# Kernel tuning notes

Hardware: AMD Instinct MI355X
Metric: run time of the kernel (lower is better)

Reference implementation:

```python
import jax, jax.numpy as jnp
import numpy as np

# Model dims (must match init_kwargs / input_specs)
D = 64          # hidden_dims
L = 2           # num_layer
R = 50          # num_relation
N_RAW = 20000   # num_nodes (module uses num_nodes+1 internally, node 0 = padding)
N = N_RAW + 1
A = 6           # max_arity
E = 30000       # num hyperedges
B = 4           # batch size
C = 500         # candidates per query (1 true + negatives, all differ in one slot)
ARITY = 4       # query arity (constant per batch, as the asserts require)
FEAT = 2 * D    # feature_dim = hidden_dims + input_dim
LN_EPS = 1e-5


def _sinusoidal_pos(max_arity, dim):
    # static_positional_encoding: frozen sinusoidal table, row 0 zeroed (padding)
    pos = np.arange(max_arity + 1, dtype=np.float64)[:, None]
    i = np.arange(dim, dtype=np.float64)[None, :]
    angle = pos / np.power(10000.0, (2.0 * np.floor(i / 2.0)) / dim)
    pe = np.where(np.arange(dim)[None, :] % 2 == 0, np.sin(angle), np.cos(angle))
    pe[0] = 0.0
    return jnp.asarray(pe, jnp.float32)


def setup_inputs() -> dict:
    key = jax.random.key(0)
    ks = jax.random.split(key, 16)
    # --- query batch: one corrupted slot per row, constant relation / arity per row ---
    base = jax.random.randint(ks[0], (B, A), 1, N)                       # entity ids 1..N-1
    base = base * (jnp.arange(A)[None, :] < ARITY)                       # pad slots >= arity -> node 0
    pos_corrupt = jax.random.randint(ks[1], (B,), 0, ARITY)              # which slot differs
    cand = (jnp.arange(C)[None, :] + jax.random.randint(ks[2], (B, 1), 1, N)) % (N - 1) + 1  # [B,C] distinct ids
    ent = jnp.broadcast_to(base[:, None, :], (B, C, A))
    entities_idx = jnp.where(jnp.arange(A)[None, None, :] == pos_corrupt[:, None, None],
                             cand[:, :, None], ent).astype(jnp.int64)    # [B,C,A]
    r_idx = jnp.broadcast_to(jax.random.randint(ks[3], (B, 1), 0, R), (B, C)).astype(jnp.int64)
    arity = jnp.full((B, C), ARITY, dtype=jnp.int64)
    # --- hypergraph: padded incidence lists ---
    edge_ar = jax.random.randint(ks[4], (E,), 2, A + 1)
    edge_list = (jax.random.randint(ks[5], (E, A), 1, N)
                 * (jnp.arange(A)[None, :] < edge_ar[:, None])).astype(jnp.int64)  # [E,A], 0-padded
    rel_list = jax.random.randint(ks[6], (E,), 0, R).astype(jnp.int64)
    # --- parameters ---
    sD = 1.0 / np.sqrt(D)
    sF = 1.0 / np.sqrt(FEAT)
    params = dict(
        query_emb=jax.random.normal(ks[7], (R, D), jnp.float32) * sD,
        rel_emb=jax.random.normal(ks[8], (L, R, D), jnp.float32) * sD,   # per-layer relation table (dependent=False)
        W_agg=jax.random.normal(ks[9], (L, D, D), jnp.float32) * sD,
        W_self=jax.random.normal(ks[10], (L, D, D), jnp.float32) * sD,
        b_lin=jnp.zeros((L, D), jnp.float32),
        ln_g=jnp.ones((L, D), jnp.float32),
        ln_b=jnp.zeros((L, D), jnp.float32),
        W1=jax.random.normal(ks[11], (FEAT, FEAT), jnp.float32) * sF,
        b1=jnp.zeros((FEAT,), jnp.float32),
        W2=jax.random.normal(ks[12], (FEAT, 1), jnp.float32) * sF,
        b2=jnp.zeros((1,), jnp.float32),
    )
    return dict(r_idx=r_idx, entities_idx=entities_idx, arity=arity,
                edge_list=edge_list, rel_list=rel_list,
                pos_table=_sinusoidal_pos(A, D), **params)


def _layer_norm(x, g, b):
    mu = x.mean(-1, keepdims=True)
    var = jnp.mean(jnp.square(x - mu), -1, keepdims=True)
    return (x - mu) * jax.lax.rsqrt(var + LN_EPS) * g + b


def reference(r_idx, entities_idx, arity, edge_list, rel_list, pos_table,
              query_emb, rel_emb, W_agg, W_self, b_lin, ln_g, ln_b, W1, b1, W2, b2):
    all_idx = jnp.transpose(entities_idx, (0, 2, 1))                 # [B,A,C]
    mask_for_diff = jnp.all(all_idx[:, :, :1] == all_idx, axis=-1)   # [B,A] True = slot constant
    pos_search = jnp.argmax(~mask_for_diff, axis=1)                  # [B] corrupted slot
    query = query_emb[r_idx[:, 0]]                                   # [B,D]

    rng = jnp.arange(A)
    valid = rng[None, :] < arity[:, :1]                              # [B,A]
    result = (valid & (rng[None, :] != pos_search[:, None])).astype(all_idx.dtype)  # [B,A]
    idx_ws = all_idx[:, :, 0] * result                               # [B,A] node ids (0 = skip)
    b_ix = jnp.arange(r_idx.shape[0])

    # init: scatter-add relation query + positional encodings onto the query entities
    init = jnp.zeros((r_idx.shape[0], N, D), jnp.float32)
    init = init.at[b_ix[:, None], idx_ws].add(
        jnp.broadcast_to(query[:, None, :], (r_idx.shape[0], A, D)))
    pos_src = pos_table[result * (rng + 1)[None, :]]                 # [B,A,D]
    init = init.at[b_ix[:, None], idx_ws].add(pos_src)
    init = init.at[:, 0, :].set(0.0)                                 # padding node stays 0

    ev = (edge_list != 0)                                            # [E,A] valid slots
    pos_e = pos_table[jnp.arange(1, A + 1)[None, :] * ev]            # [E,A,D] (pos_table[0]=0)
    evf = ev[None, :, :, None].astype(jnp.float32)

    layer_input = init
    for l in range(L):
        h_e = layer_input[:, edge_list]                              # [B,E,A,D] gather
        r_e = rel_emb[l][rel_list]                                   # [E,D]
        m = (h_e + pos_e[None]) * r_e[None, :, None, :] * evf        # per-slot message factor
        msg = (m.sum(axis=2, keepdims=True) - m) * evf               # sum over other slots j != i
        agg = jnp.zeros_like(layer_input).at[:, edge_list].add(msg)  # scatter-add to nodes
        agg = agg.at[:, 0, :].set(0.0)
        out = agg @ W_agg[l] + layer_input @ W_self[l] + b_lin[l]
        out = _layer_norm(out, ln_g[l], ln_b[l])                     # (dropout = identity at eval)
        hidden = jax.nn.relu(out)
        layer_input = hidden + layer_input                           # short_cut residual

    # gather candidate rows (exactly one differing slot per batch row -> jit-friendly)
    cand = jnp.take_along_axis(all_idx, pos_search[:, None, None], axis=1)[:, 0, :]  # [B,C]
    feat_nodes = layer_input[b_ix[:, None], cand]                    # [B,C,D]
    feat = jnp.concatenate(
        [feat_nodes, jnp.broadcast_to(query[:, None, :], feat_nodes.shape)], axis=-1)  # [B,C,2D]
    score = (jax.nn.relu(feat @ W1 + b1) @ W2 + b2)[..., 0]          # [B,C]
    return score
```

## Files before the change

### kernel.cpp

```cpp
#include <hip/hip_runtime.h>

#define D_ 64
#define L_ 2
#define R_ 50
#define N_ 20001
#define A_ 6
#define E_ 30000
#define B_ 4
#define C_ 500
#define FEAT_ 128
#define SC_CAP 8192
#define DCAP 64

__device__ __forceinline__ float rlane(float v, int k) {
  return __builtin_bit_cast(float, __builtin_amdgcn_readlane(__builtin_bit_cast(int, v), k));
}
__device__ __forceinline__ float wave_sum(float v) {
#pragma unroll
  for (int off = 32; off; off >>= 1) v += __shfl_xor(v, off);
  return v;
}
__device__ __forceinline__ float sel6(float p0, float p1, float p2, float p3,
                                      float p4, float p5, int a) {
  float r = p0;
  r = (a == 1) ? p1 : r; r = (a == 2) ? p2 : r; r = (a == 3) ? p3 : r;
  r = (a == 4) ? p4 : r; r = (a == 5) ? p5 : r;
  return r;
}


#define ZQUADS 15007

__global__ void zero_kernel(float4* __restrict__ z) {
  int i = blockIdx.x * blockDim.x + threadIdx.x;
  if (i < ZQUADS) z[i] = make_float4(0.f, 0.f, 0.f, 0.f);
}


#define IB_INIT 4
#define IB_EMASK ((E_ + 255) / 256)
#define IB_BUCKET ((E_ * A_ + 255) / 256)
#define IB_BLOCKS (IB_INIT + IB_EMASK + IB_BUCKET)

__global__ __launch_bounds__(256) void init_bucket_kernel(
    const int* __restrict__ r_idx, const int* __restrict__ ents,
    const int* __restrict__ arity, const float* __restrict__ pos_table,
    const float* __restrict__ query_emb, const int* __restrict__ edge_list,
    int* __restrict__ seednode, float* __restrict__ seedvec,
    int* __restrict__ dirtyA, int* __restrict__ dirty_n, int* __restrict__ meta,
    int* __restrict__ deg, int* __restrict__ bucket, int* __restrict__ emask) {
  __shared__ int diff[A_];
  int bid = blockIdx.x, t = threadIdx.x;
  if (bid < IB_INIT) {
    int b = bid;
    if (t < A_) diff[t] = 0;
    __syncthreads();
#pragma unroll
    for (int a = 0; a < A_; ++a) {
      int v0 = ents[(b * C_) * A_ + a];
      int dd = 0;
      for (int c = t; c < C_; c += 256) dd |= (ents[(b * C_ + c) * A_ + a] != v0);
      if (dd) diff[a] = 1;
    }
    __syncthreads();
    int ps = 0;
    for (int a = A_ - 1; a >= 0; --a) if (diff[a]) ps = a;
    int qr = r_idx[b * C_];
    if (t == 0) { meta[b] = ps; meta[B_ + b] = qr; }
    int ar = arity[b * C_];
    int lane = t & 63;
    for (int a = (t >> 6); a < A_; a += 4) {
      int slot = b * A_ + a;
      if (a < ar && a != ps) {
        int n = ents[(b * C_) * A_ + a];
        seedvec[slot * D_ + lane] = query_emb[qr * D_ + lane] + pos_table[(a + 1) * D_ + lane];
        if (lane == 0) {
          seednode[slot] = n;
          atomicOr(&dirtyA[n], 1 << b);
          atomicOr(&dirty_n[n], 1 << b);
        }
      } else {
        if (lane == 0) seednode[slot] = 0;
      }
    }
  } else if (bid < IB_INIT + IB_EMASK) {
    int e = (bid - IB_INIT) * 256 + t;
    if (e < E_) {
      int msk = 0;
#pragma unroll
      for (int a = 0; a < A_; ++a)
        if (edge_list[e * A_ + a]) msk |= 1 << a;
      emask[e] = msk;
    }
  } else {
    int i = (bid - IB_INIT - IB_EMASK) * 256 + t;
    if (i < E_ * A_) {
      int n = edge_list[i];
      if (n) {
        int slot = atomicAdd(&deg[n], 1);
        if (slot < DCAP) bucket[n * DCAP + slot] = i;
      }
    }
  }
}


#define MAIN_BLOCKS ((N_ + 31) / 32)
#define EPS_BLOCKS ((E_ + 3) / 4)

__global__ __launch_bounds__(256) void main_eps_kernel(
    const int* __restrict__ deg, const int* __restrict__ bucket,
    const int* __restrict__ edge_list, const int* __restrict__ rel_list,
    const int* __restrict__ emask,
    const float* __restrict__ pos_table, const float* __restrict__ rel_emb_l,
    float* __restrict__ H1,
    const float* __restrict__ Wa, const float* __restrict__ bl_,
    const float* __restrict__ g_, const float* __restrict__ be_,
    const int* __restrict__ dirtyA, int* __restrict__ dirty_n,
    const int* __restrict__ seednode, const float* __restrict__ seedvec,
    float* __restrict__ Scorr, unsigned short* __restrict__ emap,
    int* __restrict__ ctrs) {
  __shared__ float A_lds[32 * 68];
  __shared__ float B_lds[64 * 64];
  int t = threadIdx.x;
  int wv = t >> 6, l = t & 63;

  if (blockIdx.x >= MAIN_BLOCKS) {
    int e = (blockIdx.x - MAIN_BLOCKS) * 4 + wv;
    if (e >= E_) return;
    int mem[A_];
    int m = 0;
#pragma unroll
    for (int a = 0; a < A_; ++a) {
      mem[a] = edge_list[e * A_ + a];
      if (mem[a]) m |= dirtyA[mem[a]];
    }
    if (l == 0) *reinterpret_cast<unsigned long long*>(&emap[e * B_]) = 0ull;
    if (!m) return;
#pragma unroll
    for (int a = 0; a < A_; ++a)
      if (l == a && mem[a]) atomicOr(&dirty_n[mem[a]], m);
    float rel = rel_emb_l[rel_list[e] * D_ + l];
#pragma unroll
    for (int b = 0; b < B_; ++b) {
      if ((m >> b) & 1) {
        float s = 0.f;
#pragma unroll
        for (int a = 0; a < A_; ++a) {
          if (mem[a]) {
#pragma unroll
            for (int j = 0; j < A_; ++j) {
              int sl = b * A_ + j;
              if (seednode[sl] == mem[a]) s += seedvec[sl * D_ + l];
            }
          }
        }
        int slot = 0;
        if (l == 0) slot = atomicAdd(&ctrs[1], 1);
        slot = __shfl(slot, 0);
        if (slot < SC_CAP) {
          Scorr[slot * D_ + l] = rel * s;
          if (l == 0) emap[e * B_ + b] = (unsigned short)(slot + 1);
        }
      }
    }
    return;
  }

  int m0 = blockIdx.x * 32;
  int ty = t >> 4, tx = t & 15;

  float pv0 = pos_table[1 * D_ + l], pv1 = pos_table[2 * D_ + l];
  float pv2 = pos_table[3 * D_ + l], pv3 = pos_table[4 * D_ + l];
  float pv4 = pos_table[5 * D_ + l], pv5 = pos_table[6 * D_ + l];

#pragma unroll
  for (int it = 0; it < 4; ++it) {
    int idx = t + 256 * it;
    reinterpret_cast<float4*>(B_lds)[idx] = reinterpret_cast<const float4*>(Wa)[idx];
  }

  for (int q = 0; q < 8; ++q) {
    int li = wv * 8 + q;
    int n = m0 + li;
    float aggv = 0.f;
    if (n < N_) {
      int dg = __builtin_amdgcn_readfirstlane(deg[n]);
      int base = n * DCAP;
      for (int p = 0; p < dg; p += 8) {
        int cnt = dg - p;
        int idx8[8];
#pragma unroll
        for (int u = 0; u < 8; ++u) idx8[u] = (u < cnt) ? bucket[base + p + u] : -1;
#pragma unroll
        for (int u = 0; u < 8; ++u) {
          if (idx8[u] >= 0) {
            int e = idx8[u] / 6, a = idx8[u] - e * 6;
            int msk = emask[e];
            float rel = rel_emb_l[rel_list[e] * D_ + l];
            float possum = 0.f;
            possum += (msk & 1) ? pv0 : 0.f;
            possum += (msk & 2) ? pv1 : 0.f;
            possum += (msk & 4) ? pv2 : 0.f;
            possum += (msk & 8) ? pv3 : 0.f;
            possum += (msk & 16) ? pv4 : 0.f;
            possum += (msk & 32) ? pv5 : 0.f;
            float pa = sel6(pv0, pv1, pv2, pv3, pv4, pv5, a);
            aggv = fmaf(rel, possum - pa, aggv);
          }
        }
      }
    }
    A_lds[li * 68 + l] = aggv;
  }
  __syncthreads();

  float acc[2][4];
  float4 bl4 = *reinterpret_cast<const float4*>(&bl_[tx * 4]);
#pragma unroll
  for (int i = 0; i < 2; ++i) {
    acc[i][0] = bl4.x; acc[i][1] = bl4.y; acc[i][2] = bl4.z; acc[i][3] = bl4.w;
  }
#pragma unroll 8
  for (int k = 0; k < 64; ++k) {
    float4 b4 = *reinterpret_cast<const float4*>(&B_lds[k * 64 + tx * 4]);
    float a0 = A_lds[(ty * 2 + 0) * 68 + k];
    float a1 = A_lds[(ty * 2 + 1) * 68 + k];
    acc[0][0] = fmaf(a0, b4.x, acc[0][0]); acc[0][1] = fmaf(a0, b4.y, acc[0][1]);
    acc[0][2] = fmaf(a0, b4.z, acc[0][2]); acc[0][3] = fmaf(a0, b4.w, acc[0][3]);
    acc[1][0] = fmaf(a1, b4.x, acc[1][0]); acc[1][1] = fmaf(a1, b4.y, acc[1][1]);
    acc[1][2] = fmaf(a1, b4.z, acc[1][2]); acc[1][3] = fmaf(a1, b4.w, acc[1][3]);
  }
  __syncthreads();
#pragma unroll
  for (int i = 0; i < 2; ++i) {
    float4 v = make_float4(acc[i][0], acc[i][1], acc[i][2], acc[i][3]);
    *reinterpret_cast<float4*>(&A_lds[(ty * 2 + i) * 68 + tx * 4]) = v;
  }
  __syncthreads();

  float g = g_[l], be = be_[l];
#pragma unroll 4
  for (int rr = 0; rr < 8; ++rr) {
    int r = wv * 8 + rr;
    int n = m0 + r;
    float x = A_lds[r * 68 + l];
    float mu = wave_sum(x) * (1.f / 64.f);
    float dx = x - mu;
    float var = wave_sum(dx * dx) * (1.f / 64.f);
    float y = dx * rsqrtf(var + 1e-5f) * g + be;
    if (n < N_) H1[n * D_ + l] = fmaxf(y, 0.f);
  }
}


#define CORR_BLOCKS ((N_ + 3) / 4)
#define SB1_BLOCKS ((E_ + 3) / 4)

__global__ __launch_bounds__(256) void corr_sb1_kernel(
    const int* __restrict__ deg, const int* __restrict__ bucket,
    const int* __restrict__ edge_list, const int* __restrict__ rel_list,
    const int* __restrict__ emask,
    const float* __restrict__ pos_table,
    const float* __restrict__ rel0, const float* __restrict__ rel1,
    const float* __restrict__ Scorr, const unsigned short* __restrict__ emap,
    const int* __restrict__ dirty_n,
    const int* __restrict__ seednode, const float* __restrict__ seedvec,
    const float* __restrict__ H1,
    int* __restrict__ cmap, float* __restrict__ Hcorr,
    float* __restrict__ SB1, int* __restrict__ edirty,
    const float* __restrict__ Wa, const float* __restrict__ Ws,
    const float* __restrict__ bl_, const float* __restrict__ g_,
    const float* __restrict__ be_, int* __restrict__ ctrs) {
  int t = threadIdx.x;
  int wv = t >> 6, lane = t & 63;

  if (blockIdx.x >= CORR_BLOCKS) {
    int e = (blockIdx.x - CORR_BLOCKS) * 4 + wv;
    if (e >= E_) return;
    int mem[A_];
#pragma unroll
    for (int a = 0; a < A_; ++a) mem[a] = edge_list[e * A_ + a];
    int ed = 0;
    float s = 0.f;
#pragma unroll
    for (int a = 0; a < A_; ++a) {
      if (mem[a]) {
        ed |= dirty_n[mem[a]];
        s += H1[mem[a] * D_ + lane] + pos_table[(a + 1) * D_ + lane];
      }
    }
    float rel = rel1[rel_list[e] * D_ + lane];
    SB1[e * D_ + lane] = rel * s;
    if (lane == 0) edirty[e] = ed;
    return;
  }

  __shared__ float WaL[64 * 64];
  __shared__ float WsL[64 * 64];
  int n = blockIdx.x * 4 + wv;
  int m = (n < N_) ? dirty_n[n] : 0;
  if (__syncthreads_or(m) == 0) return;
#pragma unroll
  for (int it = 0; it < 4; ++it) {
    int idx = t + 256 * it;
    reinterpret_cast<float4*>(WaL)[idx] = reinterpret_cast<const float4*>(Wa)[idx];
    reinterpret_cast<float4*>(WsL)[idx] = reinterpret_cast<const float4*>(Ws)[idx];
  }
  __syncthreads();
  if (!m) return;

  float pv0 = pos_table[1 * D_ + lane], pv1 = pos_table[2 * D_ + lane];
  float pv2 = pos_table[3 * D_ + lane], pv3 = pos_table[4 * D_ + lane];
  float pv4 = pos_table[5 * D_ + lane], pv5 = pos_table[6 * D_ + lane];

  int slot = 0;
  if (lane == 0) slot = atomicAdd(&ctrs[2], 1);
  slot = __shfl(slot, 0);
  if (lane == 0) cmap[n] = slot;

  float blv = bl_[lane], gv = g_[lane], bev = be_[lane];
  int dg = deg[n];
  int base = n * DCAP;
  float ss0 = 0.f, ss1 = 0.f, ss2 = 0.f, ss3 = 0.f;
  float rs = 0.f, ps = 0.f;
  for (int p = 0; p < dg; ++p) {
    int ii = bucket[base + p];
    int e = ii / 6, a = ii - e * 6;
    int msk = emask[e];
    float rel = rel0[rel_list[e] * D_ + lane];
    float possum = 0.f;
    possum += (msk & 1) ? pv0 : 0.f;
    possum += (msk & 2) ? pv1 : 0.f;
    possum += (msk & 4) ? pv2 : 0.f;
    possum += (msk & 8) ? pv3 : 0.f;
    possum += (msk & 16) ? pv4 : 0.f;
    possum += (msk & 32) ? pv5 : 0.f;
    float base_v = rel * possum;
    rs += rel;
    ps = fmaf(rel, sel6(pv0, pv1, pv2, pv3, pv4, pv5, a), ps);
    if ((m >> 0) & 1) { int ei = emap[e * B_ + 0]; ss0 += base_v + (ei ? Scorr[(ei - 1) * D_ + lane] : 0.f); }
    if ((m >> 1) & 1) { int ei = emap[e * B_ + 1]; ss1 += base_v + (ei ? Scorr[(ei - 1) * D_ + lane] : 0.f); }
    if ((m >> 2) & 1) { int ei = emap[e * B_ + 2]; ss2 += base_v + (ei ? Scorr[(ei - 1) * D_ + lane] : 0.f); }
    if ((m >> 3) & 1) { int ei = emap[e * B_ + 3]; ss3 += base_v + (ei ? Scorr[(ei - 1) * D_ + lane] : 0.f); }
  }
#pragma unroll
  for (int b = 0; b < B_; ++b) {
    if ((m >> b) & 1) {
      float ssb = (b == 0) ? ss0 : (b == 1) ? ss1 : (b == 2) ? ss2 : ss3;
      float hv = 0.f;
#pragma unroll
      for (int j = 0; j < A_; ++j) {
        int sl = b * A_ + j;
        if (seednode[sl] == n) hv += seedvec[sl * D_ + lane];
      }
      float aggv = ssb - hv * rs - ps;
      float out0 = blv, out1 = 0.f;
#pragma unroll
      for (int k = 0; k < 64; k += 2) {
        out0 = fmaf(rlane(aggv, k), WaL[k * 64 + lane], out0);
        out0 = fmaf(rlane(hv, k), WsL[k * 64 + lane], out0);
        out1 = fmaf(rlane(aggv, k + 1), WaL[(k + 1) * 64 + lane], out1);
        out1 = fmaf(rlane(hv, k + 1), WsL[(k + 1) * 64 + lane], out1);
      }
      float out = out0 + out1;
      float mu = wave_sum(out) * (1.f / 64.f);
      float dx = out - mu;
      float var = wave_sum(dx * dx) * (1.f / 64.f);
      float y = dx * rsqrtf(var + 1e-5f) * gv + bev;
      Hcorr[(slot * B_ + b) * D_ + lane] = fmaxf(y, 0.f) + hv;
    }
  }
}


__global__ __launch_bounds__(256) void cand_kernel(
    const int* __restrict__ ents, const int* __restrict__ meta,
    const int* __restrict__ deg, const int* __restrict__ bucket,
    const int* __restrict__ edge_list, const int* __restrict__ rel_list,
    const float* __restrict__ pos_table, const float* __restrict__ rel_emb_l,
    const float* __restrict__ H1, const float* __restrict__ Hcorr,
    const int* __restrict__ cmap, const int* __restrict__ dirty_n,
    const float* __restrict__ SB1, const int* __restrict__ edirty,
    const float* __restrict__ query_emb,
    const float* __restrict__ Wa, const float* __restrict__ Ws,
    const float* __restrict__ bl_, const float* __restrict__ g_,
    const float* __restrict__ be_,
    const float* __restrict__ W1, const float* __restrict__ b1,
    const float* __restrict__ W2, const float* __restrict__ b2,
    float* __restrict__ out) {
  __shared__ float WaL[64 * 64];
  __shared__ float WsL[64 * 64];
  int t = threadIdx.x;
#pragma unroll
  for (int it = 0; it < 4; ++it) {
    int idx = t + 256 * it;
    reinterpret_cast<float4*>(WaL)[idx] = reinterpret_cast<const float4*>(Wa)[idx];
    reinterpret_cast<float4*>(WsL)[idx] = reinterpret_cast<const float4*>(Ws)[idx];
  }
  __syncthreads();
  int w = blockIdx.x * 4 + (t >> 6);
  int lane = t & 63;
  if (w >= B_ * C_) return;
  int b = w / C_;
  int c = w - b * C_;
  int psn = meta[b];
  int qr = meta[B_ + b];
  int n = ents[(b * C_ + c) * A_ + psn];

  float pv0 = pos_table[1 * D_ + lane], pv1 = pos_table[2 * D_ + lane];
  float pv2 = pos_table[3 * D_ + lane], pv3 = pos_table[4 * D_ + lane];
  float pv4 = pos_table[5 * D_ + lane], pv5 = pos_table[6 * D_ + lane];

  float h1v = H1[n * D_ + lane];
  if ((dirty_n[n] >> b) & 1) h1v = Hcorr[(cmap[n] * B_ + b) * D_ + lane];

  int dg = __builtin_amdgcn_readfirstlane(deg[n]);
  int base = n * DCAP;
  float ss = 0.f, rs = 0.f, ps = 0.f;
  for (int p = 0; p < dg; ++p) {
    int ii = bucket[base + p];
    int e = ii / 6, a = ii - e * 6;
    float sb = SB1[e * D_ + lane];
    float rel = rel_emb_l[rel_list[e] * D_ + lane];
    int ed = edirty[e];
    if ((ed >> b) & 1) {
      float sdelta = 0.f;
#pragma unroll
      for (int a2 = 0; a2 < A_; ++a2) {
        int m2 = edge_list[e * A_ + a2];
        if (m2 && ((dirty_n[m2] >> b) & 1))
          sdelta += Hcorr[(cmap[m2] * B_ + b) * D_ + lane] - H1[m2 * D_ + lane];
      }
      sb = fmaf(rel, sdelta, sb);
    }
    ss += sb;
    rs += rel;
    ps = fmaf(rel, sel6(pv0, pv1, pv2, pv3, pv4, pv5, a), ps);
  }
  float aggv = ss - h1v * rs - ps;

  float out0 = bl_[lane], out1 = 0.f;
#pragma unroll
  for (int k = 0; k < 64; k += 2) {
    out0 = fmaf(rlane(aggv, k), WaL[k * 64 + lane], out0);
    out0 = fmaf(rlane(h1v, k), WsL[k * 64 + lane], out0);
    out1 = fmaf(rlane(aggv, k + 1), WaL[(k + 1) * 64 + lane], out1);
    out1 = fmaf(rlane(h1v, k + 1), WsL[(k + 1) * 64 + lane], out1);
  }
  float outv = out0 + out1;
  float mu = wave_sum(outv) * (1.f / 64.f);
  float dx = outv - mu;
  float var = wave_sum(dx * dx) * (1.f / 64.f);
  float y = dx * rsqrtf(var + 1e-5f) * g_[lane] + be_[lane];
  float h2v = fmaxf(y, 0.f) + h1v;

  float qv = query_emb[qr * D_ + lane];
  float h0a = b1[lane], h0b = 0.f;
  float h1a = b1[D_ + lane], h1b = 0.f;
#pragma unroll
  for (int k = 0; k < 64; k += 2) {
    float f0 = rlane(h2v, k), f1 = rlane(h2v, k + 1);
    h0a = fmaf(f0, W1[k * FEAT_ + lane], h0a);
    h1a = fmaf(f0, W1[k * FEAT_ + D_ + lane], h1a);
    h0b = fmaf(f1, W1[(k + 1) * FEAT_ + lane], h0b);
    h1b = fmaf(f1, W1[(k + 1) * FEAT_ + D_ + lane], h1b);
  }
#pragma unroll
  for (int k = 0; k < 64; k += 2) {
    float q0 = rlane(qv, k), q1 = rlane(qv, k + 1);
    h0a = fmaf(q0, W1[(D_ + k) * FEAT_ + lane], h0a);
    h1a = fmaf(q0, W1[(D_ + k) * FEAT_ + D_ + lane], h1a);
    h0b = fmaf(q1, W1[(D_ + k + 1) * FEAT_ + lane], h0b);
    h1b = fmaf(q1, W1[(D_ + k + 1) * FEAT_ + D_ + lane], h1b);
  }
  float hid0 = h0a + h0b, hid1 = h1a + h1b;
  float accs = fmaxf(hid0, 0.f) * W2[lane] + fmaxf(hid1, 0.f) * W2[D_ + lane];
  accs = wave_sum(accs);
  if (lane == 0) out[w] = accs + b2[0];
}


extern "C" void kernel_launch(void* const* d_in, const int* in_sizes, int n_in,
                              void* d_out, int out_size, void* d_ws, size_t ws_size,
                              hipStream_t stream) {
  const int* r_idx = (const int*)d_in[0];
  const int* ents = (const int*)d_in[1];
  const int* arity = (const int*)d_in[2];
  const int* edge_list = (const int*)d_in[3];
  const int* rel_list = (const int*)d_in[4];
  const float* pos_table = (const float*)d_in[5];
  const float* query_emb = (const float*)d_in[6];
  const float* rel_emb = (const float*)d_in[7];
  const float* W_agg = (const float*)d_in[8];
  const float* W_self = (const float*)d_in[9];
  const float* b_lin = (const float*)d_in[10];
  const float* ln_g = (const float*)d_in[11];
  const float* ln_b = (const float*)d_in[12];
  const float* W1 = (const float*)d_in[13];
  const float* b1 = (const float*)d_in[14];
  const float* W2 = (const float*)d_in[15];
  const float* b2 = (const float*)d_in[16];
  float* out = (float*)d_out;

  char* ws = (char*)d_ws;
  float* H1      = (float*)(ws + 0);
  float* Hcorr   = (float*)(ws + 5120512);
  float* Scorr   = (float*)(ws + 25601536);
  int* cmap      = (int*)(ws + 27698688);
  int* seednode  = (int*)(ws + 27778816);
  float* seedvec = (float*)(ws + 27778912);
  int* meta      = (int*)(ws + 27785056);
  int* emask     = (int*)(ws + 27785216);
  unsigned short* emap = (unsigned short*)(ws + 27905216);
  int* bucket    = (int*)(ws + 28145280);
  const size_t Z = 33265536;
  int* deg       = (int*)(ws + Z);
  int* dirtyA    = (int*)(ws + Z + 80016);
  int* dirty_n   = (int*)(ws + Z + 160032);
  int* ctrs      = (int*)(ws + Z + 240048);
  const size_t ZBYTES = 240112;
  float* SB1     = (float*)(ws + 33600000);
  int* edirty    = (int*)(ws + 41280000);
  if (ws_size < 41400016) return;

  const float* rel0 = rel_emb;
  const float* rel1 = rel_emb + R_ * D_;

  zero_kernel<<<(ZQUADS + 255) / 256, 256, 0, stream>>>((float4*)(ws + Z));

  init_bucket_kernel<<<IB_BLOCKS, 256, 0, stream>>>(
      r_idx, ents, arity, pos_table, query_emb, edge_list,
      seednode, seedvec, dirtyA, dirty_n, meta, deg, bucket, emask);

  main_eps_kernel<<<MAIN_BLOCKS + EPS_BLOCKS, 256, 0, stream>>>(
      deg, bucket, edge_list, rel_list, emask, pos_table, rel0, H1,
      W_agg, b_lin, ln_g, ln_b,
      dirtyA, dirty_n, seednode, seedvec, Scorr, emap, ctrs);

  corr_sb1_kernel<<<CORR_BLOCKS + SB1_BLOCKS, 256, 0, stream>>>(
      deg, bucket, edge_list, rel_list, emask, pos_table, rel0, rel1,
      Scorr, emap, dirty_n, seednode, seedvec, H1,
      cmap, Hcorr, SB1, edirty,
      W_agg, W_self, b_lin, ln_g, ln_b, ctrs);

  cand_kernel<<<(B_ * C_ + 3) / 4, 256, 0, stream>>>(
      ents, meta, deg, bucket, edge_list, rel_list, pos_table, rel1,
      H1, Hcorr, cmap, dirty_n, SB1, edirty, query_emb,
      W_agg + D_ * D_, W_self + D_ * D_, b_lin + D_, ln_g + D_, ln_b + D_,
      W1, b1, W2, b2, out);

  (void)in_sizes; (void)n_in; (void)out_size;
}
```

Measured before the change: 113.2 us.

## Replace dense edge and node scans with compacted dirty edge/node worklists

Instead of launching one wave per hyperedge to test whether it touches a seed node, a single block walks the incidence buckets of the seed nodes and builds a deduplicated edge list. Newly dirtied nodes are also appended to a node list, so the correction stage runs over that list with a small fixed grid rather than one block per node. This removes many thousands of mostly idle waves and their reads. In exchange the edge-building step runs serially in one block, emap moves into the zeroed region, and the fixed list caps could truncate work if exceeded.

Measured after the change: 217.9 us. 92.5% more time.

```diff
diff --git a/kernel.cpp b/kernel.cpp
--- a/kernel.cpp
+++ b/kernel.cpp
@@ -1,7 +1,6 @@
 #include <hip/hip_runtime.h>
 
 #define D_ 64
-#define L_ 2
 #define R_ 50
 #define N_ 20001
 #define A_ 6
@@ -11,6 +10,8 @@
 #define FEAT_ 128
 #define SC_CAP 8192
 #define DCAP 64
+#define ELIST_CAP 4096
+#define NLIST_CAP 16384
 
 __device__ __forceinline__ float rlane(float v, int k) {
   return __builtin_bit_cast(float, __builtin_amdgcn_readlane(__builtin_bit_cast(int, v), k));
@@ -29,7 +30,7 @@
 }
 
 
-#define ZQUADS 15007
+#define ZQUADS 37508
 
 __global__ void zero_kernel(float4* __restrict__ z) {
   int i = blockIdx.x * blockDim.x + threadIdx.x;
@@ -48,7 +49,8 @@
     const float* __restrict__ query_emb, const int* __restrict__ edge_list,
     int* __restrict__ seednode, float* __restrict__ seedvec,
     int* __restrict__ dirtyA, int* __restrict__ dirty_n, int* __restrict__ meta,
-    int* __restrict__ deg, int* __restrict__ bucket, int* __restrict__ emask) {
+    int* __restrict__ deg, int* __restrict__ bucket, int* __restrict__ emask,
+    int* __restrict__ nlist, int* __restrict__ ctrs) {
   __shared__ int diff[A_];
   int bid = blockIdx.x, t = threadIdx.x;
   if (bid < IB_INIT) {
@@ -77,7 +79,11 @@
         if (lane == 0) {
           seednode[slot] = n;
           atomicOr(&dirtyA[n], 1 << b);
-          atomicOr(&dirty_n[n], 1 << b);
+          int old = atomicOr(&dirty_n[n], 1 << b);
+          if (old == 0) {
+            int s3 = atomicAdd(&ctrs[2], 1);
+            if (s3 < NLIST_CAP) nlist[s3] = n;
+          }
         }
       } else {
         if (lane == 0) seednode[slot] = 0;
@@ -106,7 +112,6 @@
 
 
 #define MAIN_BLOCKS ((N_ + 31) / 32)
-#define EPS_BLOCKS ((E_ + 3) / 4)
 
 __global__ __launch_bounds__(256) void main_eps_kernel(
     const int* __restrict__ deg, const int* __restrict__ bucket,
@@ -119,60 +124,86 @@
     const int* __restrict__ dirtyA, int* __restrict__ dirty_n,
     const int* __restrict__ seednode, const float* __restrict__ seedvec,
     float* __restrict__ Scorr, unsigned short* __restrict__ emap,
+    int* __restrict__ eflag, int* __restrict__ elist, int* __restrict__ nlist,
     int* __restrict__ ctrs) {
   __shared__ float A_lds[32 * 68];
   __shared__ float B_lds[64 * 64];
+  __shared__ int ecS;
   int t = threadIdx.x;
   int wv = t >> 6, l = t & 63;
-
-  if (blockIdx.x >= MAIN_BLOCKS) {
-    int e = (blockIdx.x - MAIN_BLOCKS) * 4 + wv;
-    if (e >= E_) return;
-    int mem[A_];
-    int m = 0;
-#pragma unroll
-    for (int a = 0; a < A_; ++a) {
-      mem[a] = edge_list[e * A_ + a];
-      if (mem[a]) m |= dirtyA[mem[a]];
-    }
-    if (l == 0) *reinterpret_cast<unsigned long long*>(&emap[e * B_]) = 0ull;
-    if (!m) return;
-#pragma unroll
-    for (int a = 0; a < A_; ++a)
-      if (l == a && mem[a]) atomicOr(&dirty_n[mem[a]], m);
-    float rel = rel_emb_l[rel_list[e] * D_ + l];
-#pragma unroll
-    for (int b = 0; b < B_; ++b) {
-      if ((m >> b) & 1) {
-        float s = 0.f;
-#pragma unroll
-        for (int a = 0; a < A_; ++a) {
-          if (mem[a]) {
-#pragma unroll
-            for (int j = 0; j < A_; ++j) {
-              int sl = b * A_ + j;
-              if (seednode[sl] == mem[a]) s += seedvec[sl * D_ + l];
-            }
-          }
-        }
-        int slot = 0;
-        if (l == 0) slot = atomicAdd(&ctrs[1], 1);
-        slot = __shfl(slot, 0);
-        if (slot < SC_CAP) {
-          Scorr[slot * D_ + l] = rel * s;
-          if (l == 0) emap[e * B_ + b] = (unsigned short)(slot + 1);
-        }
-      }
-    }
-    return;
-  }
-
-  int m0 = blockIdx.x * 32;
-  int ty = t >> 4, tx = t & 15;
 
   float pv0 = pos_table[1 * D_ + l], pv1 = pos_table[2 * D_ + l];
   float pv2 = pos_table[3 * D_ + l], pv3 = pos_table[4 * D_ + l];
   float pv4 = pos_table[5 * D_ + l], pv5 = pos_table[6 * D_ + l];
+
+  if (blockIdx.x >= MAIN_BLOCKS) {
+    for (int idx = t; idx < B_ * A_ * DCAP; idx += 256) {
+      int slot = idx / DCAP, p = idx - slot * DCAP;
+      int n = seednode[slot];
+      if (n) {
+        int dgn = deg[n]; dgn = (dgn > DCAP) ? DCAP : dgn;
+        if (p < dgn) {
+          int e = bucket[n * DCAP + p] / 6;
+          if (atomicOr(&eflag[e], 1) == 0) {
+            int s2 = atomicAdd(&ctrs[0], 1);
+            if (s2 < ELIST_CAP) elist[s2] = e;
+          }
+        }
+      }
+    }
+    __syncthreads();
+    if (t == 0) ecS = atomicAdd(&ctrs[0], 0);
+    __syncthreads();
+    int ec = ecS; if (ec > ELIST_CAP) ec = ELIST_CAP;
+    for (int i = wv; i < ec; i += 4) {
+      int e = elist[i];
+      int mem[A_];
+      int m = 0;
+#pragma unroll
+      for (int a = 0; a < A_; ++a) {
+        mem[a] = edge_list[e * A_ + a];
+        if (mem[a]) m |= dirtyA[mem[a]];
+      }
+#pragma unroll
+      for (int a = 0; a < A_; ++a) {
+        if (l == a && mem[a]) {
+          int old = atomicOr(&dirty_n[mem[a]], m);
+          if (old == 0) {
+            int s3 = atomicAdd(&ctrs[2], 1);
+            if (s3 < NLIST_CAP) nlist[s3] = mem[a];
+          }
+        }
+      }
+      float rel = rel_emb_l[rel_list[e] * D_ + l];
+#pragma unroll
+      for (int b = 0; b < B_; ++b) {
+        if ((m >> b) & 1) {
+          float s = 0.f;
+#pragma unroll
+          for (int a = 0; a < A_; ++a) {
+            if (mem[a]) {
+#pragma unroll
+              for (int j = 0; j < A_; ++j) {
+                int sl = b * A_ + j;
+                if (seednode[sl] == mem[a]) s += seedvec[sl * D_ + l];
+              }
+            }
+          }
+          int slot = 0;
+          if (l == 0) slot = atomicAdd(&ctrs[1], 1);
+          slot = __shfl(slot, 0);
+          if (slot < SC_CAP) {
+            Scorr[slot * D_ + l] = rel * s;
+            if (l == 0) emap[e * B_ + b] = (unsigned short)(slot + 1);
+          }
+        }
+      }
+    }
+    return;
+  }
+
+  int m0 = blockIdx.x * 32;
+  int ty = t >> 4, tx = t & 15;
 
 #pragma unroll
   for (int it = 0; it < 4; ++it) {
@@ -254,7 +285,7 @@
 }
 
 
-#define CORR_BLOCKS ((N_ + 3) / 4)
+#define CORRB 64
 #define SB1_BLOCKS ((E_ + 3) / 4)
 
 __global__ __launch_bounds__(256) void corr_sb1_kernel(
@@ -269,14 +300,19 @@
     const float* __restrict__ H1,
     int* __restrict__ cmap, float* __restrict__ Hcorr,
     float* __restrict__ SB1, int* __restrict__ edirty,
+    const int* __restrict__ nlist,
     const float* __restrict__ Wa, const float* __restrict__ Ws,
     const float* __restrict__ bl_, const float* __restrict__ g_,
     const float* __restrict__ be_, int* __restrict__ ctrs) {
   int t = threadIdx.x;
   int wv = t >> 6, lane = t & 63;
 
-  if (blockIdx.x >= CORR_BLOCKS) {
-    int e = (blockIdx.x - CORR_BLOCKS) * 4 + wv;
+  float pv0 = pos_table[1 * D_ + lane], pv1 = pos_table[2 * D_ + lane];
+  float pv2 = pos_table[3 * D_ + lane], pv3 = pos_table[4 * D_ + lane];
+  float pv4 = pos_table[5 * D_ + lane], pv5 = pos_table[6 * D_ + lane];
+
+  if (blockIdx.x >= CORRB) {
+    int e = (blockIdx.x - CORRB) * 4 + wv;
     if (e >= E_) return;
     int mem[A_];
 #pragma unroll
@@ -287,7 +323,8 @@
     for (int a = 0; a < A_; ++a) {
       if (mem[a]) {
         ed |= dirty_n[mem[a]];
-        s += H1[mem[a] * D_ + lane] + pos_table[(a + 1) * D_ + lane];
+        float pa = sel6(pv0, pv1, pv2, pv3, pv4, pv5, a);
+        s += H1[mem[a] * D_ + lane] + pa;
       }
     }
     float rel = rel1[rel_list[e] * D_ + lane];
@@ -298,9 +335,6 @@
 
   __shared__ float WaL[64 * 64];
   __shared__ float WsL[64 * 64];
-  int n = blockIdx.x * 4 + wv;
-  int m = (n < N_) ? dirty_n[n] : 0;
-  if (__syncthreads_or(m) == 0) return;
 #pragma unroll
   for (int it = 0; it < 4; ++it) {
     int idx = t + 256 * it;
@@ -308,67 +342,67 @@
     reinterpret_cast<float4*>(WsL)[idx] = reinterpret_cast<const float4*>(Ws)[idx];
   }
   __syncthreads();
-  if (!m) return;
-
-  float pv0 = pos_table[1 * D_ + lane], pv1 = pos_table[2 * D_ + lane];
-  float pv2 = pos_table[3 * D_ + lane], pv3 = pos_table[4 * D_ + lane];
-  float pv4 = pos_table[5 * D_ + lane], pv5 = pos_table[6 * D_ + lane];
-
-  int slot = 0;
-  if (lane == 0) slot = atomicAdd(&ctrs[2], 1);
-  slot = __shfl(slot, 0);
-  if (lane == 0) cmap[n] = slot;
-
-  float blv = bl_[lane], gv = g_[lane], bev = be_[lane];
-  int dg = deg[n];
-  int base = n * DCAP;
-  float ss0 = 0.f, ss1 = 0.f, ss2 = 0.f, ss3 = 0.f;
-  float rs = 0.f, ps = 0.f;
-  for (int p = 0; p < dg; ++p) {
-    int ii = bucket[base + p];
-    int e = ii / 6, a = ii - e * 6;
-    int msk = emask[e];
-    float rel = rel0[rel_list[e] * D_ + lane];
-    float possum = 0.f;
-    possum += (msk & 1) ? pv0 : 0.f;
-    possum += (msk & 2) ? pv1 : 0.f;
-    possum += (msk & 4) ? pv2 : 0.f;
-    possum += (msk & 8) ? pv3 : 0.f;
-    possum += (msk & 16) ? pv4 : 0.f;
-    possum += (msk & 32) ? pv5 : 0.f;
-    float base_v = rel * possum;
-    rs += rel;
-    ps = fmaf(rel, sel6(pv0, pv1, pv2, pv3, pv4, pv5, a), ps);
-    if ((m >> 0) & 1) { int ei = emap[e * B_ + 0]; ss0 += base_v + (ei ? Scorr[(ei - 1) * D_ + lane] : 0.f); }
-    if ((m >> 1) & 1) { int ei = emap[e * B_ + 1]; ss1 += base_v + (ei ? Scorr[(ei - 1) * D_ + lane] : 0.f); }
-    if ((m >> 2) & 1) { int ei = emap[e * B_ + 2]; ss2 += base_v + (ei ? Scorr[(ei - 1) * D_ + lane] : 0.f); }
-    if ((m >> 3) & 1) { int ei = emap[e * B_ + 3]; ss3 += base_v + (ei ? Scorr[(ei - 1) * D_ + lane] : 0.f); }
-  }
-#pragma unroll
-  for (int b = 0; b < B_; ++b) {
-    if ((m >> b) & 1) {
-      float ssb = (b == 0) ? ss0 : (b == 1) ? ss1 : (b == 2) ? ss2 : ss3;
-      float hv = 0.f;
-#pragma unroll
-      for (int j = 0; j < A_; ++j) {
-        int sl = b * A_ + j;
-        if (seednode[sl] == n) hv += seedvec[sl * D_ + lane];
-      }
-      float aggv = ssb - hv * rs - ps;
-      float out0 = blv, out1 = 0.f;
-#pragma unroll
-      for (int k = 0; k < 64; k += 2) {
-        out0 = fmaf(rlane(aggv, k), WaL[k * 64 + lane], out0);
-        out0 = fmaf(rlane(hv, k), WsL[k * 64 + lane], out0);
-        out1 = fmaf(rlane(aggv, k + 1), WaL[(k + 1) * 64 + lane], out1);
-        out1 = fmaf(rlane(hv, k + 1), WsL[(k + 1) * 64 + lane], out1);
-      }
-      float out = out0 + out1;
-      float mu = wave_sum(out) * (1.f / 64.f);
-      float dx = out - mu;
-      float var = wave_sum(dx * dx) * (1.f / 64.f);
-      float y = dx * rsqrtf(var + 1e-5f) * gv + bev;
-      Hcorr[(slot * B_ + b) * D_ + lane] = fmaxf(y, 0.f) + hv;
+
+  int cntn = ctrs[2]; if (cntn > NLIST_CAP) cntn = NLIST_CAP;
+  for (int i = blockIdx.x * 4 + wv; i < cntn; i += CORRB * 4) {
+    int n = nlist[i];
+    int m = dirty_n[n];
+    int slot = 0;
+    if (lane == 0) slot = atomicAdd(&ctrs[3], 1);
+    slot = __shfl(slot, 0);
+    if (lane == 0) cmap[n] = slot;
+
+    float blv = bl_[lane], gv = g_[lane], bev = be_[lane];
+    int dg = deg[n];
+    int base = n * DCAP;
+    float ss0 = 0.f, ss1 = 0.f, ss2 = 0.f, ss3 = 0.f;
+    float rs = 0.f, ps = 0.f;
+    for (int p = 0; p < dg; ++p) {
+      int ii = bucket[base + p];
+      int e = ii / 6, a = ii - e * 6;
+      int msk = emask[e];
+      float rel = rel0[rel_list[e] * D_ + lane];
+      float possum = 0.f;
+      possum += (msk & 1) ? pv0 : 0.f;
+      possum += (msk & 2) ? pv1 : 0.f;
+      possum += (msk & 4) ? pv2 : 0.f;
+      possum += (msk & 8) ? pv3 : 0.f;
+      possum += (msk & 16) ? pv4 : 0.f;
+      possum += (msk & 32) ? pv5 : 0.f;
+      float base_v = rel * possum;
+      rs += rel;
+      ps = fmaf(rel, sel6(pv0, pv1, pv2, pv3, pv4, pv5, a), ps);
+      if ((m >> 0) & 1) { int ei = emap[e * B_ + 0]; ss0 += base_v + (ei ? Scorr[(ei - 1) * D_ + lane] : 0.f); }
+      if ((m >> 1) & 1) { int ei = emap[e * B_ + 1]; ss1 += base_v + (ei ? Scorr[(ei - 1) * D_ + lane] : 0.f); }
+      if ((m >> 2) & 1) { int ei = emap[e * B_ + 2]; ss2 += base_v + (ei ? Scorr[(ei - 1) * D_ + lane] : 0.f); }
+      if ((m >> 3) & 1) { int ei = emap[e * B_ + 3]; ss3 += base_v + (ei ? Scorr[(ei - 1) * D_ + lane] : 0.f); }
+    }
+#pragma unroll
+    for (int b = 0; b < B_; ++b) {
+      if ((m >> b) & 1) {
+        float ssb = (b == 0) ? ss0 : (b == 1) ? ss1 : (b == 2) ? ss2 : ss3;
+        float hv = 0.f;
+#pragma unroll
+        for (int j = 0; j < A_; ++j) {
+          int sl = b * A_ + j;
+          if (seednode[sl] == n) hv += seedvec[sl * D_ + lane];
+        }
+        float aggv = ssb - hv * rs - ps;
+        float out0 = blv, out1 = 0.f;
+#pragma unroll
+        for (int k = 0; k < 64; k += 2) {
+          out0 = fmaf(rlane(aggv, k), WaL[k * 64 + lane], out0);
+          out0 = fmaf(rlane(hv, k), WsL[k * 64 + lane], out0);
+          out1 = fmaf(rlane(aggv, k + 1), WaL[(k + 1) * 64 + lane], out1);
+          out1 = fmaf(rlane(hv, k + 1), WsL[(k + 1) * 64 + lane], out1);
+        }
+        float o = out0 + out1;
+        float mu = wave_sum(o) * (1.f / 64.f);
+        float dx = o - mu;
+        float var = wave_sum(dx * dx) * (1.f / 64.f);
+        float y = dx * rsqrtf(var + 1e-5f) * gv + bev;
+        Hcorr[(slot * B_ + b) * D_ + lane] = fmaxf(y, 0.f) + hv;
+      }
     }
   }
 }
@@ -512,17 +546,20 @@
   float* seedvec = (float*)(ws + 27778912);
   int* meta      = (int*)(ws + 27785056);
   int* emask     = (int*)(ws + 27785216);
-  unsigned short* emap = (unsigned short*)(ws + 27905216);
-  int* bucket    = (int*)(ws + 28145280);
-  const size_t Z = 33265536;
+  int* bucket    = (int*)(ws + 27905216);
+  int* elist     = (int*)(ws + 33025472);
+  int* nlist     = (int*)(ws + 33041856);
+  float* SB1     = (float*)(ws + 33107392);
+  int* edirty    = (int*)(ws + 40787392);
+  const size_t Z = 40907392;
   int* deg       = (int*)(ws + Z);
   int* dirtyA    = (int*)(ws + Z + 80016);
   int* dirty_n   = (int*)(ws + Z + 160032);
   int* ctrs      = (int*)(ws + Z + 240048);
-  const size_t ZBYTES = 240112;
-  float* SB1     = (float*)(ws + 33600000);
-  int* edirty    = (int*)(ws + 41280000);
-  if (ws_size < 41400016) return;
+  int* eflag     = (int*)(ws + Z + 240112);
+  unsigned short* emap = (unsigned short*)(ws + Z + 360112);
+  const size_t ZBYTES = 600128;
+  if (ws_size < Z + ZBYTES) return;
 
   const float* rel0 = rel_emb;
   const float* rel1 = rel_emb + R_ * D_;
@@ -531,17 +568,18 @@
 
   init_bucket_kernel<<<IB_BLOCKS, 256, 0, stream>>>(
       r_idx, ents, arity, pos_table, query_emb, edge_list,
-      seednode, seedvec, dirtyA, dirty_n, meta, deg, bucket, emask);
-
-  main_eps_kernel<<<MAIN_BLOCKS + EPS_BLOCKS, 256, 0, stream>>>(
+      seednode, seedvec, dirtyA, dirty_n, meta, deg, bucket, emask,
+      nlist, ctrs);
+
+  main_eps_kernel<<<MAIN_BLOCKS + 1, 256, 0, stream>>>(
       deg, bucket, edge_list, rel_list, emask, pos_table, rel0, H1,
       W_agg, b_lin, ln_g, ln_b,
-      dirtyA, dirty_n, seednode, seedvec, Scorr, emap, ctrs);
-
-  corr_sb1_kernel<<<CORR_BLOCKS + SB1_BLOCKS, 256, 0, stream>>>(
+      dirtyA, dirty_n, seednode, seedvec, Scorr, emap, eflag, elist, nlist, ctrs);
+
+  corr_sb1_kernel<<<CORRB + SB1_BLOCKS, 256, 0, stream>>>(
       deg, bucket, edge_list, rel_list, emask, pos_table, rel0, rel1,
       Scorr, emap, dirty_n, seednode, seedvec, H1,
-      cmap, Hcorr, SB1, edirty,
+      cmap, Hcorr, SB1, edirty, nlist,
       W_agg, W_self, b_lin, ln_g, ln_b, ctrs);
 
   cand_kernel<<<(B_ * C_ + 3) / 4, 256, 0, stream>>>(
```
